# Kernel tuning notes

Measured on AMD Instinct MI355X. Metric: run time of the kernel, lower is better.

## Reference

```python
import jax, jax.numpy as jnp
import numpy as np


def _lstm_bi(x, wih, whh, b):
    # x: [B,T,D]; wih: [2,D,4H]; whh: [2,H,4H]; b: [2,4H]. PyTorch gate order i,f,g,o.
    def run(xs, wi, wh, bb):
        B, H = xs.shape[1], wh.shape[0]
        def step(carry, xt):
            h, c = carry
            g = xt @ wi + h @ wh + bb
            i, f, gg, o = jnp.split(g, 4, axis=-1)
            c = jax.nn.sigmoid(f) * c + jax.nn.sigmoid(i) * jnp.tanh(gg)
            h = jax.nn.sigmoid(o) * jnp.tanh(c)
            return (h, c), h
        z0 = jnp.zeros((B, H), xs.dtype)
        _, hs = jax.lax.scan(step, (z0, z0), xs)
        return hs
    xs = jnp.swapaxes(x, 0, 1)  # [T,B,D]
    hf = run(xs, wih[0], whh[0], b[0])
    hb = run(xs[::-1], wih[1], whh[1], b[1])[::-1]
    return jnp.swapaxes(jnp.concatenate([hf, hb], axis=-1), 0, 1)


def _norm_thr(att, thr):
    # sum-normalize, threshold-sparsify, renormalize (PSP core)
    att = att / (jnp.sum(att, -1, keepdims=True) + 1e-8)
    att = jnp.where(att > thr, att, jnp.zeros_like(att))
    return att / (jnp.sum(att, -1, keepdims=True) + 1e-8)


def _ln(x, g, b):
    mu = jnp.mean(x, -1, keepdims=True)
    var = jnp.mean(jnp.square(x - mu), -1, keepdims=True)
    return (x - mu) / jnp.sqrt(var + 1e-6) * g + b


def _forward(audio, video, thr_val, fa_w1, fa_w2, av_aw, av_ab, av_vw, av_vb,
             av_v2w, av_gw, av_hw, fv_w1, fv_w2, la_wih, la_whh, la_b,
             lv_wih, lv_whh, lv_b, vL1, vL2, aL1, aL2, vfc, afc, ln_g, ln_b, L1w, L2w):
    bs, T = audio.shape[0], audio.shape[1]
    fa = (audio @ fa_w1) @ fa_w2                          # [B,T,128]
    vf = video.reshape(bs, T, -1, video.shape[-1])        # [B,T,49,512]
    # AVGA audio-guided visual attention
    v_h = jax.nn.relu(vf @ av_vw + av_vb)                 # [B,T,49,512]
    a_h = jax.nn.relu(fa @ av_aw + av_ab)                 # [B,T,512]
    content = v_h @ av_v2w + (a_h @ av_gw)[..., None]     # [B,T,49,49]
    z = jnp.squeeze(jnp.tanh(content) @ av_hw, -1)        # [B,T,49]
    alpha = jax.nn.softmax(z, -1)
    video_t = jnp.einsum('btp,btpd->btd', alpha, vf)      # [B,T,512]
    video_t = (video_t @ fv_w1) @ fv_w2                   # [B,T,128]
    # bidirectional LSTMs
    lstm_a = _lstm_bi(fa, la_wih, la_whh, la_b)           # [B,T,256]
    lstm_v = _lstm_bi(video_t, lv_wih, lv_whh, lv_b)      # [B,T,256]
    # PSP (eval mode: dropout is identity)
    v_b1 = jax.nn.relu(lstm_v @ vL1)
    v_b2 = jax.nn.relu(lstm_v @ vL2)
    a_b1 = jax.nn.relu(lstm_a @ aL1)
    a_b2 = jax.nn.relu(lstm_a @ aL2)
    scale = 1.0 / jnp.sqrt(jnp.asarray(v_b2.shape[-1], v_b2.dtype))
    att = jax.nn.relu(jnp.einsum('bvd,bad->bva', v_b2, a_b1) * scale)  # v->a raw
    att_v2a = _norm_thr(att, thr_val)
    att_a2v = _norm_thr(jnp.swapaxes(att, 1, 2), thr_val)
    v_psp = lstm_v + jnp.einsum('bva,bad->bvd', att_v2a, a_b2)
    a_psp = lstm_a + jnp.einsum('bav,bvd->bad', att_a2v, v_b1)
    v_psp = _ln(jax.nn.relu(v_psp @ vfc), ln_g, ln_b)
    a_psp = _ln(jax.nn.relu(a_psp @ afc), ln_g, ln_b)
    fuse = 0.5 * (v_psp + a_psp)
    vn = v_psp / jnp.maximum(jnp.linalg.norm(v_psp, axis=-1, keepdims=True), 1e-12)
    an = a_psp / jnp.maximum(jnp.linalg.norm(a_psp, axis=-1, keepdims=True), 1e-12)
    cross_att = jnp.sum(vn * an, -1)                      # [B,T]
    out = jax.nn.relu(fuse @ L1w) @ L2w                   # [B,T,29]
    return (fuse, out, cross_att)


def setup_inputs() -> dict:
    key = jax.random.key(0)
    ks = iter(jax.random.split(key, 40))
    def w(*shape):
        fan_in = shape[-2] if len(shape) > 1 else shape[-1]
        return jax.random.normal(next(ks), shape, jnp.float32) * (1.0 / np.sqrt(fan_in))
    B, T = 256, 10
    return dict(
        audio=jax.random.normal(next(ks), (B, T, 128), jnp.float32),
        video=jax.random.normal(next(ks), (B, T, 7, 7, 512), jnp.float32),
        thr_val=jnp.float32(0.099),
        fa_w1=w(128, 256), fa_w2=w(256, 128),
        av_aw=w(128, 512), av_ab=jnp.zeros((512,), jnp.float32),
        av_vw=w(512, 512), av_vb=jnp.zeros((512,), jnp.float32),
        av_v2w=w(512, 49), av_gw=w(512, 49), av_hw=w(49, 1),
        fv_w1=w(512, 256), fv_w2=w(256, 128),
        la_wih=w(2, 128, 512), la_whh=w(2, 128, 512), la_b=jnp.zeros((2, 512), jnp.float32),
        lv_wih=w(2, 128, 512), lv_whh=w(2, 128, 512), lv_b=jnp.zeros((2, 512), jnp.float32),
        vL1=w(256, 256), vL2=w(256, 256), aL1=w(256, 256), aL2=w(256, 256),
        vfc=w(256, 256), afc=w(256, 256),
        ln_g=jnp.ones((256,), jnp.float32), ln_b=jnp.zeros((256,), jnp.float32),
        L1w=w(256, 64), L2w=w(64, 29),
    )


def reference(audio, video, thr_val, fa_w1, fa_w2, av_aw, av_ab, av_vw, av_vb,
              av_v2w, av_gw, av_hw, fv_w1, fv_w2, la_wih, la_whh, la_b,
              lv_wih, lv_whh, lv_b, vL1, vL2, aL1, aL2, vfc, afc, ln_g, ln_b, L1w, L2w):
    return _forward(audio, video, thr_val, fa_w1, fa_w2, av_aw, av_ab, av_vw, av_vb,
                    av_v2w, av_gw, av_hw, fv_w1, fv_w2, la_wih, la_whh, la_b,
                    lv_wih, lv_whh, lv_b, vL1, vL2, aL1, aL2, vfc, afc, ln_g, ln_b, L1w, L2w)
```

## Files before the change

kernel.cpp:

```cpp
#include <hip/hip_runtime.h>
#include <math.h>

#define DEV __device__ __forceinline__

typedef _Float16 f16x8 __attribute__((ext_vector_type(8)));
typedef _Float16 f16x4 __attribute__((ext_vector_type(4)));
typedef float    f32x4 __attribute__((ext_vector_type(4)));

DEV float sigmoidf_(float x){ return 1.0f/(1.0f + expf(-x)); }

DEV float wred64(float x){
    #pragma unroll
    for (int off=32; off; off>>=1) x += __shfl_xor(x, off);
    return x;
}

__global__ __launch_bounds__(256) void k_prep(
    const float* __restrict__ fa_w1, const float* __restrict__ fa_w2, float* __restrict__ faW,
    const float* __restrict__ fv_w1, const float* __restrict__ fv_w2, float* __restrict__ fvW,
    const float* __restrict__ av_vw, _Float16* __restrict__ Bh, _Float16* __restrict__ Bl,
    const float* __restrict__ v2w, _Float16* __restrict__ Wh, _Float16* __restrict__ Wl)
{
    int bid = blockIdx.x, t = threadIdx.x;
    if (bid < 64){
        int idx = bid*256+t; int m = idx>>7, n = idx&127;
        float acc=0.f;
        for (int k=0;k<256;k++) acc += fa_w1[m*256+k]*fa_w2[k*128+n];
        faW[idx]=acc;
    } else if (bid < 320){
        int idx = (bid-64)*256+t; int m = idx>>7, n = idx&127;
        float acc=0.f;
        for (int k=0;k<256;k++) acc += fv_w1[m*256+k]*fv_w2[k*128+n];
        fvW[idx]=acc;
    } else if (bid < 1344){
        int o = (bid-320)*256+t;
        int j = o & 7, l16 = (o>>3)&15, kg = (o>>7)&3, nf = (o>>9)&31, kt = o>>14;
        int k = kt*32 + kg*8 + j, n = nf*16 + l16;
        float x = av_vw[(size_t)k*512 + n];
        _Float16 h = (_Float16)x;
        Bh[o] = h; Bl[o] = (_Float16)(x - (float)h);
    } else {
        int o = (bid-1344)*256+t;
        int j = o & 7, l16 = (o>>3)&15, kg = (o>>7)&3, qf = (o>>9)&3, kbg = o>>11;
        int k = kbg*32 + kg*8 + j, q = qf*16 + l16;
        float x = (q < 49) ? v2w[(size_t)k*49 + q] : 0.f;
        _Float16 h = (_Float16)x;
        Wh[o] = h; Wl[o] = (_Float16)(x - (float)h);
    }
}

__global__ __launch_bounds__(256) void k_faga(
    const float* __restrict__ audio, const float* __restrict__ faW,
    const float* __restrict__ av_aw, const float* __restrict__ av_ab,
    const float* __restrict__ av_gw, float* __restrict__ fa, float* __restrict__ gGA)
{
    int b0 = blockIdx.x*4; int t = threadIdx.x;
    __shared__ float sau[4][128], sfa[4][128], sah[4][512];
    for (int i=t;i<512;i+=256){ int bt=i>>7,k=i&127; sau[bt][k]=audio[(size_t)(b0+bt)*128+k]; }
    __syncthreads();
    for (int u=0;u<2;u++){
        int i=t+u*256, bt=i>>7, n=i&127;
        float acc=0.f;
        for (int k4=0;k4<32;k4++){
            float4 x4=*(const float4*)&sau[bt][k4*4];
            acc+=x4.x*faW[(k4*4)*128+n]+x4.y*faW[(k4*4+1)*128+n]
                +x4.z*faW[(k4*4+2)*128+n]+x4.w*faW[(k4*4+3)*128+n];
        }
        sfa[bt][n]=acc; fa[(size_t)(b0+bt)*128+n]=acc;
    }
    __syncthreads();
    for (int u=0;u<2;u++){
        int n=t+u*256;
        float bv=av_ab[n];
        float acc[4]={bv,bv,bv,bv};
        for (int k4=0;k4<32;k4++){
            float w0=av_aw[(k4*4)*512+n], w1=av_aw[(k4*4+1)*512+n],
                  w2=av_aw[(k4*4+2)*512+n], w3=av_aw[(k4*4+3)*512+n];
            #pragma unroll
            for (int bt=0;bt<4;bt++){
                float4 x4=*(const float4*)&sfa[bt][k4*4];
                acc[bt]+=x4.x*w0+x4.y*w1+x4.z*w2+x4.w*w3;
            }
        }
        #pragma unroll
        for (int bt=0;bt<4;bt++) sah[bt][n]=fmaxf(acc[bt],0.f);
    }
    __syncthreads();
    if (t<196){
        int bt=t/49, q=t-bt*49;
        float acc=0.f;
        for (int k=0;k<512;k++) acc+=sah[bt][k]*av_gw[k*49+q];
        gGA[(size_t)(b0+bt)*49+q]=acc;
    }
}

DEV void cvt4_(float4 v, f16x4& hv, f16x4& lv){
    hv[0]=(_Float16)v.x; lv[0]=(_Float16)(v.x-(float)hv[0]);
    hv[1]=(_Float16)v.y; lv[1]=(_Float16)(v.y-(float)hv[1]);
    hv[2]=(_Float16)v.z; lv[2]=(_Float16)(v.z-(float)hv[2]);
    hv[3]=(_Float16)v.w; lv[3]=(_Float16)(v.w-(float)hv[3]);
}

#define MFMA16(a,b,c) __builtin_amdgcn_mfma_f32_16x16x32_f16(a,b,c,0,0,0)

__global__ __launch_bounds__(256,2) void k_avga_fused(
    const float* __restrict__ video,
    const _Float16* __restrict__ Bh, const _Float16* __restrict__ Bl,
    const float* __restrict__ bias,
    const _Float16* __restrict__ Wh, const _Float16* __restrict__ Wl,
    const float* __restrict__ gGA,
    const float* __restrict__ hw,
    float* __restrict__ vT)
{
    __shared__ __align__(16) char smem[67072];
    int bt = blockIdx.x;
    int t = threadIdx.x;
    int lane = t & 63, w = t >> 6;
    int l16 = lane & 15, lq = lane >> 4;
    int lb = lane * 16;

    int am = t >> 3, ak = (t & 7) * 4;
    int aoff1 = ((am>>4)*4 + (ak>>3))*256 + (am&15)*16 + (ak&7)*2;
    int am2 = am + 32;
    int aoff2 = ((am2>>4)*4 + (ak>>3))*256 + (am2&15)*16 + (ak&7)*2;
    size_t r1 = (size_t)bt*49 + am;  if (r1 > 125439) r1 = 125439;
    size_t r2 = (size_t)bt*49 + am2; if (r2 > 125439) r2 = 125439;
    const float* Arow1 = video + r1*512 + ak;
    const float* Arow2 = video + r2*512 + ak;

    const f32x4 vzero = {0.f,0.f,0.f,0.f};
    f32x4 acc[4][8];
    #pragma unroll
    for (int p=0;p<4;p++)
        #pragma unroll
        for (int q=0;q<8;q++) acc[p][q] = vzero;

    float4 pa0, pa1;
    pa0 = *(const float4*)(Arow1);
    pa1 = *(const float4*)(Arow2);
    {
        f16x4 hv, lv;
        char* h = &smem[0];
        cvt4_(pa0, hv, lv);
        *(f16x4*)(h + aoff1) = hv; *(f16x4*)(h + 4096 + aoff1) = lv;
        cvt4_(pa1, hv, lv);
        *(f16x4*)(h + aoff2) = hv; *(f16x4*)(h + 4096 + aoff2) = lv;
    }
    __syncthreads();

    for (int kt = 0; kt < 16; ++kt){
        int cur = kt & 1;
        bool more = (kt < 15);
        if (more){
            pa0 = *(const float4*)(Arow1 + (kt+1)*32);
            pa1 = *(const float4*)(Arow2 + (kt+1)*32);
        }
        const char* aB = &smem[cur*8192];
        f16x8 ah[4], al[4];
        #pragma unroll
        for (int p=0;p<4;p++){
            ah[p] = *(const f16x8*)(aB + p*1024 + lb);
            al[p] = *(const f16x8*)(aB + 4096 + p*1024 + lb);
        }
        #pragma unroll
        for (int q=0;q<8;q++){
            size_t bo = (size_t)kt*16384 + (size_t)(w*8 + q)*512 + lane*8;
            f16x8 bh  = *(const f16x8*)(Bh + bo);
            f16x8 bl2 = *(const f16x8*)(Bl + bo);
            #pragma unroll
            for (int p=0;p<4;p++){
                acc[p][q] = MFMA16(ah[p], bh,  acc[p][q]);
                acc[p][q] = MFMA16(ah[p], bl2, acc[p][q]);
                acc[p][q] = MFMA16(al[p], bh,  acc[p][q]);
            }
        }
        if (more){
            char* h = &smem[(cur^1)*8192];
            f16x4 hv, lv;
            cvt4_(pa0, hv, lv);
            *(f16x4*)(h + aoff1) = hv; *(f16x4*)(h + 4096 + aoff1) = lv;
            cvt4_(pa1, hv, lv);
            *(f16x4*)(h + aoff2) = hv; *(f16x4*)(h + 4096 + aoff2) = lv;
        }
        __syncthreads();
    }

    float bv[8];
    #pragma unroll
    for (int q=0;q<8;q++) bv[q] = bias[w*128 + q*16 + l16];

    char* vh = &smem[16384 + w*8192];
    f32x4 cacc[4][4];
    #pragma unroll
    for (int p=0;p<4;p++)
        #pragma unroll
        for (int qf=0;qf<4;qf++) cacc[p][qf] = vzero;

    #pragma unroll
    for (int c=0;c<4;c++){
        #pragma unroll
        for (int p=0;p<4;p++)
            #pragma unroll
            for (int qq=0;qq<2;qq++){
                int q = c*2 + qq;
                int offbase = p*1024 + (qq*2 + (l16>>3))*256 + (l16&7)*2;
                #pragma unroll
                for (int r=0;r<4;r++){
                    float x = fmaxf(acc[p][q][r] + bv[q], 0.f);
                    _Float16 hh = (_Float16)x;
                    _Float16 ll = (_Float16)(x - (float)hh);
                    int off = offbase + (lq*4 + r)*16;
                    *(_Float16*)(vh + off)        = hh;
                    *(_Float16*)(vh + 4096 + off) = ll;
                }
            }
        int kbg = w*4 + c;
        f16x8 vhh[4], vhl[4];
        #pragma unroll
        for (int p=0;p<4;p++){
            vhh[p] = *(const f16x8*)(vh + p*1024 + lb);
            vhl[p] = *(const f16x8*)(vh + 4096 + p*1024 + lb);
        }
        #pragma unroll
        for (int qf=0;qf<4;qf++){
            size_t wo = (size_t)kbg*2048 + qf*512 + lane*8;
            f16x8 wh = *(const f16x8*)(Wh + wo);
            f16x8 wl = *(const f16x8*)(Wl + wo);
            #pragma unroll
            for (int p=0;p<4;p++){
                cacc[p][qf] = MFMA16(vhh[p], wh, cacc[p][qf]);
                cacc[p][qf] = MFMA16(vhh[p], wl, cacc[p][qf]);
                cacc[p][qf] = MFMA16(vhl[p], wh, cacc[p][qf]);
            }
        }
    }

    __syncthreads();
    float* pw = (float*)&smem[w*16384];
    #pragma unroll
    for (int p=0;p<4;p++)
        #pragma unroll
        for (int qf=0;qf<4;qf++)
            #pragma unroll
            for (int r=0;r<4;r++)
                pw[(p*16 + lq*4 + r)*64 + qf*16 + l16] = cacc[p][qf][r];
    __syncthreads();
    float* cb = (float*)&smem[0];
    for (int i=t; i<4096; i+=256)
        cb[i] = cb[i] + cb[4096+i] + cb[8192+i] + cb[12288+i];
    __syncthreads();

    float* szp    = (float*)&smem[65536];
    float* salpha = (float*)&smem[66560];
    if (t < 196){
        int p = t >> 2, ds = t & 3;
        float ga = gGA[(size_t)bt*49 + p];
        float part = 0.f;
        for (int q = ds*13; q < ds*13+13 && q < 49; q++)
            part += tanhf(cb[p*64 + q] + ga) * hw[q];
        szp[t] = part;
    }
    __syncthreads();
    if (t < 64){
        float z = (t<49) ? (szp[t*4]+szp[t*4+1]+szp[t*4+2]+szp[t*4+3]) : -1e30f;
        float m = z;
        #pragma unroll
        for (int off=32; off; off>>=1) m = fmaxf(m, __shfl_xor(m, off));
        float e = (t<49)? expf(z - m) : 0.f;
        float s = e;
        #pragma unroll
        for (int off=32; off; off>>=1) s += __shfl_xor(s, off);
        salpha[t] = e / s;
    }
    __syncthreads();
    const float* vb = video + (size_t)bt*49*512;
    #pragma unroll
    for (int u=0;u<2;u++){
        int d = t + u*256;
        float a0 = 0.f;
        for (int p=0;p<49;p++) a0 += salpha[p] * vb[(size_t)p*512 + d];
        vT[(size_t)bt*512 + d] = a0;
    }
}

__global__ __launch_bounds__(256) void k_xproj2(
    const float* __restrict__ vT, const float* __restrict__ fvW,
    const float* __restrict__ fa,
    const float* __restrict__ la_wih, const float* __restrict__ la_b,
    const float* __restrict__ lv_wih, const float* __restrict__ lv_b,
    float* __restrict__ xp)
{
    int b0 = blockIdx.x*8; int t = threadIdx.x;
    __shared__ float svt[8][512];
    __shared__ float sx[2][8][128];
    for (int i=t;i<4096;i+=256){ int bt=i>>9,k=i&511; svt[bt][k]=vT[(size_t)(b0+bt)*512+k]; }
    for (int i=t;i<1024;i+=256){ int bt=i>>7,k=i&127; sx[0][bt][k]=fa[(size_t)(b0+bt)*128+k]; }
    __syncthreads();
    for (int u=0;u<4;u++){
        int i=t+u*256; int bt=i>>7, n=i&127;
        float acc=0.f;
        for (int k4=0;k4<128;k4++){
            float4 x4 = *(const float4*)&svt[bt][k4*4];
            acc += x4.x*fvW[(k4*4)*128+n] + x4.y*fvW[(k4*4+1)*128+n]
                 + x4.z*fvW[(k4*4+2)*128+n] + x4.w*fvW[(k4*4+3)*128+n];
        }
        sx[1][bt][n]=acc;
    }
    __syncthreads();
    for (int c=0;c<4;c++){
        const float* wih = ((c<2)? la_wih : lv_wih) + (size_t)(c&1)*65536;
        const float* bb  = ((c<2)? la_b   : lv_b  ) + (size_t)(c&1)*512;
        for (int u=0;u<2;u++){
            int n = t + u*256;
            float bvv = bb[n];
            float acc[8];
            #pragma unroll
            for (int bt=0;bt<8;bt++) acc[bt]=bvv;
            for (int k4=0;k4<32;k4++){
                float w0=wih[(k4*4)*512+n], w1=wih[(k4*4+1)*512+n],
                      w2=wih[(k4*4+2)*512+n], w3=wih[(k4*4+3)*512+n];
                #pragma unroll
                for (int bt=0;bt<8;bt++){
                    float4 x4 = *(const float4*)&sx[c>>1][bt][k4*4];
                    acc[bt] += x4.x*w0 + x4.y*w1 + x4.z*w2 + x4.w*w3;
                }
            }
            #pragma unroll
            for (int bt=0;bt<8;bt++)
                xp[((size_t)c*2560 + b0+bt)*512 + n] = acc[bt];
        }
    }
}

__global__ __launch_bounds__(256) void k_lstm(
    const float* __restrict__ xp, const float* __restrict__ la_whh,
    const float* __restrict__ lv_whh,
    float* __restrict__ lstm_a, float* __restrict__ lstm_v)
{
    int blk = blockIdx.x;
    int c = blk >> 6;
    int chunk = blk & 63;
    int t = threadIdx.x;
    int j  = t & 127;
    int bh = t >> 7;
    const float* whh = ((c<2)? la_whh : lv_whh) + (size_t)(c&1)*128*512;
    float* outp = (c<2)? lstm_a : lstm_v;
    int dir = c & 1;

    __shared__ float hbuf[4][128];
    float cc[2] = {0.f,0.f};
    for (int i=t;i<512;i+=256) ((float*)hbuf)[i] = 0.f;
    __syncthreads();

    for (int s=0; s<10; s++){
        int tt = dir ? (9-s) : s;
        float gi[2], gf[2], gg[2], go[2];
        #pragma unroll
        for (int b=0;b<2;b++){
            int gb = chunk*4 + bh*2 + b;
            const float* xrow = xp + ((size_t)c*2560 + gb*10 + tt)*512;
            gi[b]=xrow[j]; gf[b]=xrow[128+j]; gg[b]=xrow[256+j]; go[b]=xrow[384+j];
        }
        #pragma unroll 4
        for (int k=0;k<128;k++){
            float wi = whh[k*512 + j];
            float wf = whh[k*512 + 128 + j];
            float wg = whh[k*512 + 256 + j];
            float wo = whh[k*512 + 384 + j];
            #pragma unroll
            for (int b=0;b<2;b++){
                float hk = hbuf[bh*2+b][k];
                gi[b] += hk*wi; gf[b] += hk*wf; gg[b] += hk*wg; go[b] += hk*wo;
            }
        }
        __syncthreads();
        #pragma unroll
        for (int b=0;b<2;b++){
            float i_ = sigmoidf_(gi[b]);
            float f_ = sigmoidf_(gf[b]);
            float g_ = tanhf(gg[b]);
            float o_ = sigmoidf_(go[b]);
            cc[b] = f_*cc[b] + i_*g_;
            float h_ = o_*tanhf(cc[b]);
            hbuf[bh*2+b][j] = h_;
            int gb = chunk*4 + bh*2 + b;
            outp[((size_t)gb*10 + tt)*256 + dir*128 + j] = h_;
        }
        __syncthreads();
    }
}

__global__ __launch_bounds__(256) void k_psp1(
    const float* __restrict__ lstm_a, const float* __restrict__ lstm_v,
    const float* __restrict__ vL1, const float* __restrict__ vL2,
    const float* __restrict__ aL1, const float* __restrict__ aL2,
    float* __restrict__ vb1, float* __restrict__ vb2,
    float* __restrict__ ab1, float* __restrict__ ab2)
{
    int b0 = blockIdx.x*8; int t = threadIdx.x;
    __shared__ float sa[8][256], sv[8][256];
    for (int i=t;i<2048;i+=256){
        int bt=i>>8, k=i&255;
        sa[bt][k]=lstm_a[(size_t)(b0+bt)*256+k];
        sv[bt][k]=lstm_v[(size_t)(b0+bt)*256+k];
    }
    __syncthreads();
    float a1[8],a2[8],v1[8],v2[8];
    #pragma unroll
    for (int bt=0;bt<8;bt++){ a1[bt]=0;a2[bt]=0;v1[bt]=0;v2[bt]=0; }
    for (int k4=0;k4<64;k4++){
        #pragma unroll
        for (int j=0;j<4;j++){
            int k = k4*4+j;
            float wv1 = vL1[k*256+t], wv2 = vL2[k*256+t];
            float wa1 = aL1[k*256+t], wa2 = aL2[k*256+t];
            #pragma unroll
            for (int bt=0;bt<8;bt++){
                float xv = sv[bt][k], xa = sa[bt][k];
                v1[bt]+=xv*wv1; v2[bt]+=xv*wv2;
                a1[bt]+=xa*wa1; a2[bt]+=xa*wa2;
            }
        }
    }
    #pragma unroll
    for (int bt=0;bt<8;bt++){
        size_t o = (size_t)(b0+bt)*256+t;
        vb1[o]=fmaxf(v1[bt],0.f); vb2[o]=fmaxf(v2[bt],0.f);
        ab1[o]=fmaxf(a1[bt],0.f); ab2[o]=fmaxf(a2[bt],0.f);
    }
}

__global__ __launch_bounds__(256) void k_att(
    const float* __restrict__ lstm_a, const float* __restrict__ lstm_v,
    const float* __restrict__ vb1, const float* __restrict__ vb2,
    const float* __restrict__ ab1, const float* __restrict__ ab2,
    const float* __restrict__ thrp,
    float* __restrict__ vpsp, float* __restrict__ apsp)
{
    int b = blockIdx.x, t = threadIdx.x;
    __shared__ float sV2[2560], sA1[2560], sV1[2560], sA2[2560];
    __shared__ float satt[100], s_v2a[100], s_a2v[100];
    size_t base = (size_t)b*2560;
    for (int i=t;i<2560;i+=256){
        sV2[i]=vb2[base+i]; sA1[i]=ab1[base+i];
        sV1[i]=vb1[base+i]; sA2[i]=ab2[base+i];
    }
    __syncthreads();
    if (t < 100){
        int v = t/10, a = t - v*10;
        float acc=0.f;
        for (int k=0;k<256;k++) acc += sV2[v*256+k]*sA1[a*256+k];
        satt[t] = fmaxf(acc*(1.0f/16.0f), 0.f);
    }
    __syncthreads();
    float thr = thrp[0];
    if (t < 10){
        int v = t;
        float rs=0.f; for(int a=0;a<10;a++) rs += satt[v*10+a];
        float inv = 1.f/(rs+1e-8f);
        float tmp[10]; float rs2=0.f;
        for(int a=0;a<10;a++){ float x = satt[v*10+a]*inv; x = (x>thr)?x:0.f; tmp[a]=x; rs2+=x; }
        float inv2 = 1.f/(rs2+1e-8f);
        for(int a=0;a<10;a++) s_v2a[v*10+a] = tmp[a]*inv2;
    } else if (t>=16 && t<26){
        int a = t-16;
        float cs=0.f; for(int v=0;v<10;v++) cs += satt[v*10+a];
        float inv = 1.f/(cs+1e-8f);
        float tmp[10]; float cs2=0.f;
        for(int v=0;v<10;v++){ float x = satt[v*10+a]*inv; x=(x>thr)?x:0.f; tmp[v]=x; cs2+=x; }
        float inv2 = 1.f/(cs2+1e-8f);
        for(int v=0;v<10;v++) s_a2v[a*10+v] = tmp[v]*inv2;
    }
    __syncthreads();
    for (int v=0;v<10;v++){
        float acc = lstm_v[base + v*256 + t];
        #pragma unroll
        for (int a=0;a<10;a++) acc += s_v2a[v*10+a]*sA2[a*256+t];
        vpsp[base + v*256 + t] = acc;
    }
    for (int a=0;a<10;a++){
        float acc = lstm_a[base + a*256 + t];
        #pragma unroll
        for (int v=0;v<10;v++) acc += s_a2v[a*10+v]*sV1[v*256+t];
        apsp[base + a*256 + t] = acc;
    }
}

__global__ __launch_bounds__(256) void k_fin(
    const float* __restrict__ vpsp, const float* __restrict__ apsp,
    const float* __restrict__ vfc, const float* __restrict__ afc,
    const float* __restrict__ ln_g, const float* __restrict__ ln_b,
    const float* __restrict__ L1w, const float* __restrict__ L2w,
    float* __restrict__ dout)
{
    int b0 = blockIdx.x*8;
    int t = threadIdx.x, w = t>>6, lane = t&63;
    __shared__ float sv[8][256], sa[8][256];
    __shared__ float sfu[4][256];
    __shared__ float s64b[4][64];
    for (int i=t;i<2048;i+=256){
        int bt=i>>8, k=i&255;
        sv[bt][k]=vpsp[(size_t)(b0+bt)*256+k];
        sa[bt][k]=apsp[(size_t)(b0+bt)*256+k];
    }
    __syncthreads();
    int c0 = lane*4;
    int bt0 = w*2;
    float vv[2][4], aa[2][4];
    #pragma unroll
    for (int h=0;h<2;h++)
        #pragma unroll
        for (int jj=0;jj<4;jj++){ vv[h][jj]=0.f; aa[h][jj]=0.f; }
    for (int k=0;k<256;k++){
        float4 cv = *(const float4*)&vfc[k*256+c0];
        float4 ca = *(const float4*)&afc[k*256+c0];
        float xv0 = sv[bt0][k], xv1 = sv[bt0+1][k];
        float xa0 = sa[bt0][k], xa1 = sa[bt0+1][k];
        vv[0][0]+=xv0*cv.x; vv[0][1]+=xv0*cv.y; vv[0][2]+=xv0*cv.z; vv[0][3]+=xv0*cv.w;
        vv[1][0]+=xv1*cv.x; vv[1][1]+=xv1*cv.y; vv[1][2]+=xv1*cv.z; vv[1][3]+=xv1*cv.w;
        aa[0][0]+=xa0*ca.x; aa[0][1]+=xa0*ca.y; aa[0][2]+=xa0*ca.z; aa[0][3]+=xa0*ca.w;
        aa[1][0]+=xa1*ca.x; aa[1][1]+=xa1*ca.y; aa[1][2]+=xa1*ca.z; aa[1][3]+=xa1*ca.w;
    }
    float4 g4 = *(const float4*)&ln_g[c0];
    float4 b4 = *(const float4*)&ln_b[c0];
    float gv[4]={g4.x,g4.y,g4.z,g4.w}, bb[4]={b4.x,b4.y,b4.z,b4.w};

    for (int h=0;h<2;h++){
        int row = b0 + bt0 + h;
        float xv[4], xa[4];
        #pragma unroll
        for (int jj=0;jj<4;jj++){ xv[jj]=fmaxf(vv[h][jj],0.f); xa[jj]=fmaxf(aa[h][jj],0.f); }
        float s1 = wred64(xv[0]+xv[1]+xv[2]+xv[3]);
        float s2 = wred64(xv[0]*xv[0]+xv[1]*xv[1]+xv[2]*xv[2]+xv[3]*xv[3]);
        float mu = s1*(1.f/256.f);
        float var = s2*(1.f/256.f) - mu*mu;
        float rs = 1.f/sqrtf(var+1e-6f);
        float vln[4];
        #pragma unroll
        for (int jj=0;jj<4;jj++) vln[jj] = (xv[jj]-mu)*rs*gv[jj]+bb[jj];
        s1 = wred64(xa[0]+xa[1]+xa[2]+xa[3]);
        s2 = wred64(xa[0]*xa[0]+xa[1]*xa[1]+xa[2]*xa[2]+xa[3]*xa[3]);
        mu = s1*(1.f/256.f);
        var = s2*(1.f/256.f) - mu*mu;
        rs = 1.f/sqrtf(var+1e-6f);
        float aln[4];
        #pragma unroll
        for (int jj=0;jj<4;jj++) aln[jj] = (xa[jj]-mu)*rs*gv[jj]+bb[jj];

        float fu[4];
        #pragma unroll
        for (int jj=0;jj<4;jj++){ fu[jj] = 0.5f*(vln[jj]+aln[jj]); dout[(size_t)row*256 + c0 + jj] = fu[jj]; }

        float nv2 = wred64(vln[0]*vln[0]+vln[1]*vln[1]+vln[2]*vln[2]+vln[3]*vln[3]);
        float na2 = wred64(aln[0]*aln[0]+aln[1]*aln[1]+aln[2]*aln[2]+aln[3]*aln[3]);
        float dva = wred64(vln[0]*aln[0]+vln[1]*aln[1]+vln[2]*aln[2]+vln[3]*aln[3]);
        if (lane==0){
            float nv = fmaxf(sqrtf(nv2), 1e-12f);
            float na = fmaxf(sqrtf(na2), 1e-12f);
            dout[729600 + row] = dva/(nv*na);
        }
        *(float4*)&sfu[w][c0] = make_float4(fu[0],fu[1],fu[2],fu[3]);
        float acc = 0.f;
        for (int k4=0;k4<64;k4++){
            float4 f4 = *(const float4*)&sfu[w][k4*4];
            acc += f4.x*L1w[(k4*4)*64+lane] + f4.y*L1w[(k4*4+1)*64+lane]
                 + f4.z*L1w[(k4*4+2)*64+lane] + f4.w*L1w[(k4*4+3)*64+lane];
        }
        s64b[w][lane] = fmaxf(acc, 0.f);
        if (lane < 29){
            float acc2 = 0.f;
            #pragma unroll
            for (int k=0;k<64;k++) acc2 += s64b[w][k]*L2w[k*29+lane];
            dout[655360 + (size_t)row*29 + lane] = acc2;
        }
    }
}

extern "C" void kernel_launch(void* const* d_in, const int* in_sizes, int n_in,
                              void* d_out, int out_size, void* d_ws, size_t ws_size,
                              hipStream_t stream) {
    const float* audio  = (const float*)d_in[0];
    const float* video  = (const float*)d_in[1];
    const float* thrp   = (const float*)d_in[2];
    const float* fa_w1  = (const float*)d_in[3];
    const float* fa_w2  = (const float*)d_in[4];
    const float* av_aw  = (const float*)d_in[5];
    const float* av_ab  = (const float*)d_in[6];
    const float* av_vw  = (const float*)d_in[7];
    const float* av_vb  = (const float*)d_in[8];
    const float* av_v2w = (const float*)d_in[9];
    const float* av_gw  = (const float*)d_in[10];
    const float* av_hw  = (const float*)d_in[11];
    const float* fv_w1  = (const float*)d_in[12];
    const float* fv_w2  = (const float*)d_in[13];
    const float* la_wih = (const float*)d_in[14];
    const float* la_whh = (const float*)d_in[15];
    const float* la_b   = (const float*)d_in[16];
    const float* lv_wih = (const float*)d_in[17];
    const float* lv_whh = (const float*)d_in[18];
    const float* lv_b   = (const float*)d_in[19];
    const float* vL1    = (const float*)d_in[20];
    const float* vL2    = (const float*)d_in[21];
    const float* aL1    = (const float*)d_in[22];
    const float* aL2    = (const float*)d_in[23];
    const float* vfc    = (const float*)d_in[24];
    const float* afc    = (const float*)d_in[25];
    const float* ln_g   = (const float*)d_in[26];
    const float* ln_b   = (const float*)d_in[27];
    const float* L1w    = (const float*)d_in[28];
    const float* L2w    = (const float*)d_in[29];
    float* dout = (float*)d_out;
    float* ws = (float*)d_ws;

    float* faW  = ws;
    float* fvW  = ws + 16384;
    float* fa   = ws + 81920;
    float* gGA  = ws + 409600;
    float* vT   = ws + 535040;
    float* xp   = ws + 2173440;
    float* la   = ws + 7416320;
    float* lv   = ws + 8071680;
    float* vb1  = ws + 8727040;
    float* vb2  = ws + 9382400;
    float* ab1  = ws + 10037760;
    float* ab2  = ws + 10693120;
    float* vpsp = ws + 11348480;
    float* apsp = ws + 12003840;
    _Float16* Bh = (_Float16*)(ws + 12659200);
    _Float16* Bl = (_Float16*)(ws + 12790272);
    _Float16* Wh = (_Float16*)(ws + 12921344);
    _Float16* Wl = (_Float16*)(ws + 12937728);

    k_prep<<<1472, 256, 0, stream>>>(fa_w1, fa_w2, faW, fv_w1, fv_w2, fvW,
                                     av_vw, Bh, Bl, av_v2w, Wh, Wl);
    k_faga<<<640, 256, 0, stream>>>(audio, faW, av_aw, av_ab, av_gw, fa, gGA);
    k_avga_fused<<<2560, 256, 0, stream>>>(video, Bh, Bl, av_vb, Wh, Wl,
                                           gGA, av_hw, vT);
    k_xproj2<<<320, 256, 0, stream>>>(vT, fvW, fa, la_wih, la_b, lv_wih, lv_b, xp);
    k_lstm<<<256, 256, 0, stream>>>(xp, la_whh, lv_whh, la, lv);
    k_psp1<<<320, 256, 0, stream>>>(la, lv, vL1, vL2, aL1, aL2, vb1, vb2, ab1, ab2);
    k_att<<<256, 256, 0, stream>>>(la, lv, vb1, vb2, ab1, ab2, thrp, vpsp, apsp);
    k_fin<<<320, 256, 0, stream>>>(vpsp, apsp, vfc, afc, ln_g, ln_b, L1w, L2w, dout);
}
```

Baseline: 741.6 us.

## Move small projection GEMMs to split-fp16 MFMA kernel with packed weights

Replaces the scalar FP32 projection kernels (xproj, psp1, and the fc part of fin) with a templated MFMA GEMM. It uses hi/lo fp16 splitting for near-fp32 accuracy, with weights pre-packed into MFMA fragment layout by a new prep kernel. It also cuts AVGA shared memory by reducing the 4-wave partial sums into two buffers, which allows 3 blocks per CU. This adds more kernel launches plus a weight-packing pass that runs on every call.

New measurement: 1.212 ms. +63.4%, slower.

```diff
diff --git a/kernel.cpp b/kernel.cpp
--- a/kernel.cpp
+++ b/kernel.cpp
@@ -14,6 +14,8 @@
     for (int off=32; off; off>>=1) x += __shfl_xor(x, off);
     return x;
 }
+
+#define MFMA16(a,b,c) __builtin_amdgcn_mfma_f32_16x16x32_f16(a,b,c,0,0,0)
 
 __global__ __launch_bounds__(256) void k_prep(
     const float* __restrict__ fa_w1, const float* __restrict__ fa_w2, float* __restrict__ faW,
@@ -49,6 +51,49 @@
     }
 }
 
+DEV void packone(const float* __restrict__ src, int N, int NfrTot, int nfOff,
+                 _Float16* __restrict__ Dh, _Float16* __restrict__ Dl, int o){
+    int j = o&7, l16 = (o>>3)&15, kg = (o>>7)&3;
+    int rest = o>>9;
+    int nfl = rest % (N>>4), kt = rest / (N>>4);
+    int k = kt*32 + kg*8 + j, n = nfl*16 + l16;
+    float x = src[(size_t)k*N + n];
+    _Float16 h = (_Float16)x;
+    size_t d = ((size_t)kt*NfrTot + nfOff + nfl)*512 + kg*128 + l16*8 + j;
+    Dh[d] = h; Dl[d] = (_Float16)(x - (float)h);
+}
+
+__global__ __launch_bounds__(256) void k_prep2(
+    const float* __restrict__ fvW,
+    const float* __restrict__ la_wih, const float* __restrict__ lv_wih,
+    const float* __restrict__ vL1, const float* __restrict__ vL2,
+    const float* __restrict__ aL1, const float* __restrict__ aL2,
+    const float* __restrict__ vfc, const float* __restrict__ afc,
+    _Float16* PKfv_h, _Float16* PKfv_l,
+    _Float16* PKxa_h, _Float16* PKxa_l,
+    _Float16* PKxv_h, _Float16* PKxv_l,
+    _Float16* PKvl_h, _Float16* PKvl_l,
+    _Float16* PKal_h, _Float16* PKal_l,
+    _Float16* PKvf_h, _Float16* PKvf_l,
+    _Float16* PKaf_h, _Float16* PKaf_l)
+{
+    int seg = blockIdx.x >> 8;
+    int o = (blockIdx.x & 255)*256 + threadIdx.x;
+    switch(seg){
+    case 0:  packone(fvW,            128,  8,  0, PKfv_h, PKfv_l, o); break;
+    case 1:  packone(la_wih,         512, 64,  0, PKxa_h, PKxa_l, o); break;
+    case 2:  packone(la_wih+65536,   512, 64, 32, PKxa_h, PKxa_l, o); break;
+    case 3:  packone(lv_wih,         512, 64,  0, PKxv_h, PKxv_l, o); break;
+    case 4:  packone(lv_wih+65536,   512, 64, 32, PKxv_h, PKxv_l, o); break;
+    case 5:  packone(vL1,            256, 32,  0, PKvl_h, PKvl_l, o); break;
+    case 6:  packone(vL2,            256, 32, 16, PKvl_h, PKvl_l, o); break;
+    case 7:  packone(aL1,            256, 32,  0, PKal_h, PKal_l, o); break;
+    case 8:  packone(aL2,            256, 32, 16, PKal_h, PKal_l, o); break;
+    case 9:  packone(vfc,            256, 16,  0, PKvf_h, PKvf_l, o); break;
+    default: packone(afc,            256, 16,  0, PKaf_h, PKaf_l, o); break;
+    }
+}
+
 __global__ __launch_bounds__(256) void k_faga(
     const float* __restrict__ audio, const float* __restrict__ faW,
     const float* __restrict__ av_aw, const float* __restrict__ av_ab,
@@ -101,18 +146,15 @@
     hv[3]=(_Float16)v.w; lv[3]=(_Float16)(v.w-(float)hv[3]);
 }
 
-#define MFMA16(a,b,c) __builtin_amdgcn_mfma_f32_16x16x32_f16(a,b,c,0,0,0)
-
-__global__ __launch_bounds__(256,2) void k_avga_fused(
+__global__ __launch_bounds__(256,3) void k_avga_fused(
     const float* __restrict__ video,
     const _Float16* __restrict__ Bh, const _Float16* __restrict__ Bl,
     const float* __restrict__ bias,
     const _Float16* __restrict__ Wh, const _Float16* __restrict__ Wl,
-    const float* __restrict__ gGA,
-    const float* __restrict__ hw,
+    const float* __restrict__ gGA, const float* __restrict__ hw,
     float* __restrict__ vT)
 {
-    __shared__ __align__(16) char smem[67072];
+    __shared__ __align__(16) char smem[49152];
     int bt = blockIdx.x;
     int t = threadIdx.x;
     int lane = t & 63, w = t >> 6;
@@ -236,28 +278,38 @@
     }
 
     __syncthreads();
-    float* pw = (float*)&smem[w*16384];
-    #pragma unroll
-    for (int p=0;p<4;p++)
-        #pragma unroll
-        for (int qf=0;qf<4;qf++)
-            #pragma unroll
-            for (int r=0;r<4;r++)
-                pw[(p*16 + lq*4 + r)*64 + qf*16 + l16] = cacc[p][qf][r];
-    __syncthreads();
-    float* cb = (float*)&smem[0];
-    for (int i=t; i<4096; i+=256)
-        cb[i] = cb[i] + cb[4096+i] + cb[8192+i] + cb[12288+i];
-    __syncthreads();
-
-    float* szp    = (float*)&smem[65536];
-    float* salpha = (float*)&smem[66560];
+    float* rbuf = (float*)&smem[(w&1)*16384];
+    if (w < 2){
+        #pragma unroll
+        for (int p=0;p<4;p++)
+            #pragma unroll
+            for (int qf=0;qf<4;qf++)
+                #pragma unroll
+                for (int r=0;r<4;r++)
+                    rbuf[(p*16 + lq*4 + r)*64 + qf*16 + l16] = cacc[p][qf][r];
+    }
+    __syncthreads();
+    if (w >= 2){
+        #pragma unroll
+        for (int p=0;p<4;p++)
+            #pragma unroll
+            for (int qf=0;qf<4;qf++)
+                #pragma unroll
+                for (int r=0;r<4;r++)
+                    rbuf[(p*16 + lq*4 + r)*64 + qf*16 + l16] += cacc[p][qf][r];
+    }
+    __syncthreads();
+
+    const float* cb0 = (const float*)&smem[0];
+    const float* cb1 = (const float*)&smem[16384];
+    float* szp    = (float*)&smem[32768];
+    float* salpha = (float*)&smem[33792];
     if (t < 196){
         int p = t >> 2, ds = t & 3;
         float ga = gGA[(size_t)bt*49 + p];
         float part = 0.f;
         for (int q = ds*13; q < ds*13+13 && q < 49; q++)
-            part += tanhf(cb[p*64 + q] + ga) * hw[q];
+            part += tanhf(cb0[p*64 + q] + cb1[p*64 + q] + ga) * hw[q];
         szp[t] = part;
     }
     __syncthreads();
@@ -283,58 +335,91 @@
     }
 }
 
-__global__ __launch_bounds__(256) void k_xproj2(
-    const float* __restrict__ vT, const float* __restrict__ fvW,
-    const float* __restrict__ fa,
-    const float* __restrict__ la_wih, const float* __restrict__ la_b,
-    const float* __restrict__ lv_wih, const float* __restrict__ lv_b,
-    float* __restrict__ xp)
+template<int MP, int NQ, bool BIAS, bool RELU>
+__global__ __launch_bounds__(256) void k_gemm(
+    const float* __restrict__ A, int lda,
+    const _Float16* __restrict__ Wh, const _Float16* __restrict__ Wl,
+    const float* __restrict__ bias,
+    float* __restrict__ C, int ldc,
+    int nkt, int Nfr)
 {
-    int b0 = blockIdx.x*8; int t = threadIdx.x;
-    __shared__ float svt[8][512];
-    __shared__ float sx[2][8][128];
-    for (int i=t;i<4096;i+=256){ int bt=i>>9,k=i&511; svt[bt][k]=vT[(size_t)(b0+bt)*512+k]; }
-    for (int i=t;i<1024;i+=256){ int bt=i>>7,k=i&127; sx[0][bt][k]=fa[(size_t)(b0+bt)*128+k]; }
-    __syncthreads();
-    for (int u=0;u<4;u++){
-        int i=t+u*256; int bt=i>>7, n=i&127;
-        float acc=0.f;
-        for (int k4=0;k4<128;k4++){
-            float4 x4 = *(const float4*)&svt[bt][k4*4];
-            acc += x4.x*fvW[(k4*4)*128+n] + x4.y*fvW[(k4*4+1)*128+n]
-                 + x4.z*fvW[(k4*4+2)*128+n] + x4.w*fvW[(k4*4+3)*128+n];
-        }
-        sx[1][bt][n]=acc;
-    }
-    __syncthreads();
-    for (int c=0;c<4;c++){
-        const float* wih = ((c<2)? la_wih : lv_wih) + (size_t)(c&1)*65536;
-        const float* bb  = ((c<2)? la_b   : lv_b  ) + (size_t)(c&1)*512;
-        for (int u=0;u<2;u++){
-            int n = t + u*256;
-            float bvv = bb[n];
-            float acc[8];
-            #pragma unroll
-            for (int bt=0;bt<8;bt++) acc[bt]=bvv;
-            for (int k4=0;k4<32;k4++){
-                float w0=wih[(k4*4)*512+n], w1=wih[(k4*4+1)*512+n],
-                      w2=wih[(k4*4+2)*512+n], w3=wih[(k4*4+3)*512+n];
-                #pragma unroll
-                for (int bt=0;bt<8;bt++){
-                    float4 x4 = *(const float4*)&sx[c>>1][bt][k4*4];
-                    acc[bt] += x4.x*w0 + x4.y*w1 + x4.z*w2 + x4.w*w3;
-                }
+    __shared__ __align__(16) char sA[2][MP*2048];
+    int t = threadIdx.x, lane = t&63, w = t>>6;
+    int l16 = lane&15, lq = lane>>4, lb = lane*16;
+    int row0 = blockIdx.x * (MP*16);
+    int nf0 = blockIdx.y * (4*NQ) + w*NQ;
+
+    int am = t>>3, ak = (t&7)*4;
+    int aoff = ((am>>4)*4 + (ak>>3))*256 + (am&15)*16 + (ak&7)*2;
+    const float* Arow = A + (size_t)(row0+am)*lda + ak;
+
+    const f32x4 vzero = {0.f,0.f,0.f,0.f};
+    f32x4 acc[MP][NQ];
+    #pragma unroll
+    for (int p=0;p<MP;p++)
+        #pragma unroll
+        for (int q=0;q<NQ;q++) acc[p][q] = vzero;
+
+    float4 pa = *(const float4*)(Arow);
+    {
+        f16x4 hv, lv;
+        char* h = &sA[0][0];
+        cvt4_(pa, hv, lv);
+        *(f16x4*)(h + aoff) = hv; *(f16x4*)(h + MP*1024 + aoff) = lv;
+    }
+    __syncthreads();
+
+    for (int kt = 0; kt < nkt; ++kt){
+        int cur = kt & 1;
+        bool more = (kt+1 < nkt);
+        if (more) pa = *(const float4*)(Arow + (kt+1)*32);
+        const char* aB = &sA[cur][0];
+        f16x8 ah[MP], al[MP];
+        #pragma unroll
+        for (int p=0;p<MP;p++){
+            ah[p] = *(const f16x8*)(aB + p*1024 + lb);
+            al[p] = *(const f16x8*)(aB + MP*1024 + p*1024 + lb);
+        }
+        #pragma unroll
+        for (int q=0;q<NQ;q++){
+            size_t bo = ((size_t)kt*Nfr + nf0 + q)*512 + lane*8;
+            f16x8 bh  = *(const f16x8*)(Wh + bo);
+            f16x8 bl2 = *(const f16x8*)(Wl + bo);
+            #pragma unroll
+            for (int p=0;p<MP;p++){
+                acc[p][q] = MFMA16(ah[p], bh,  acc[p][q]);
+                acc[p][q] = MFMA16(ah[p], bl2, acc[p][q]);
+                acc[p][q] = MFMA16(al[p], bh,  acc[p][q]);
             }
-            #pragma unroll
-            for (int bt=0;bt<8;bt++)
-                xp[((size_t)c*2560 + b0+bt)*512 + n] = acc[bt];
+        }
+        if (more){
+            char* h = &sA[cur^1][0];
+            f16x4 hv, lv;
+            cvt4_(pa, hv, lv);
+            *(f16x4*)(h + aoff) = hv; *(f16x4*)(h + MP*1024 + aoff) = lv;
+        }
+        __syncthreads();
+    }
+
+    #pragma unroll
+    for (int q=0;q<NQ;q++){
+        int n = (nf0+q)*16 + l16;
+        float bv = BIAS ? bias[n] : 0.f;
+        #pragma unroll
+        for (int p=0;p<MP;p++){
+            #pragma unroll
+            for (int r=0;r<4;r++){
+                float v = acc[p][q][r] + bv;
+                if (RELU) v = fmaxf(v, 0.f);
+                C[(size_t)(row0 + p*16 + lq*4 + r)*ldc + n] = v;
+            }
         }
     }
 }
 
 __global__ __launch_bounds__(256) void k_lstm(
-    const float* __restrict__ xp, const float* __restrict__ la_whh,
-    const float* __restrict__ lv_whh,
+    const float* __restrict__ xpA, const float* __restrict__ xpV,
+    const float* __restrict__ la_whh, const float* __restrict__ lv_whh,
     float* __restrict__ lstm_a, float* __restrict__ lstm_v)
 {
     int blk = blockIdx.x;
@@ -344,6 +429,7 @@
     int j  = t & 127;
     int bh = t >> 7;
     const float* whh = ((c<2)? la_whh : lv_whh) + (size_t)(c&1)*128*512;
+    const float* xpm = (c<2)? xpA : xpV;
     float* outp = (c<2)? lstm_a : lstm_v;
     int dir = c & 1;
 
@@ -358,7 +444,7 @@
         #pragma unroll
         for (int b=0;b<2;b++){
             int gb = chunk*4 + bh*2 + b;
-            const float* xrow = xp + ((size_t)c*2560 + gb*10 + tt)*512;
+            const float* xrow = xpm + ((size_t)gb*10 + tt)*1024 + dir*512;
             gi[b]=xrow[j]; gf[b]=xrow[128+j]; gg[b]=xrow[256+j]; go[b]=xrow[384+j];
         }
         #pragma unroll 4
@@ -390,50 +476,9 @@
     }
 }
 
-__global__ __launch_bounds__(256) void k_psp1(
-    const float* __restrict__ lstm_a, const float* __restrict__ lstm_v,
-    const float* __restrict__ vL1, const float* __restrict__ vL2,
-    const float* __restrict__ aL1, const float* __restrict__ aL2,
-    float* __restrict__ vb1, float* __restrict__ vb2,
-    float* __restrict__ ab1, float* __restrict__ ab2)
-{
-    int b0 = blockIdx.x*8; int t = threadIdx.x;
-    __shared__ float sa[8][256], sv[8][256];
-    for (int i=t;i<2048;i+=256){
-        int bt=i>>8, k=i&255;
-        sa[bt][k]=lstm_a[(size_t)(b0+bt)*256+k];
-        sv[bt][k]=lstm_v[(size_t)(b0+bt)*256+k];
-    }
-    __syncthreads();
-    float a1[8],a2[8],v1[8],v2[8];
-    #pragma unroll
-    for (int bt=0;bt<8;bt++){ a1[bt]=0;a2[bt]=0;v1[bt]=0;v2[bt]=0; }
-    for (int k4=0;k4<64;k4++){
-        #pragma unroll
-        for (int j=0;j<4;j++){
-            int k = k4*4+j;
-            float wv1 = vL1[k*256+t], wv2 = vL2[k*256+t];
-            float wa1 = aL1[k*256+t], wa2 = aL2[k*256+t];
-            #pragma unroll
-            for (int bt=0;bt<8;bt++){
-                float xv = sv[bt][k], xa = sa[bt][k];
-                v1[bt]+=xv*wv1; v2[bt]+=xv*wv2;
-                a1[bt]+=xa*wa1; a2[bt]+=xa*wa2;
-            }
-        }
-    }
-    #pragma unroll
-    for (int bt=0;bt<8;bt++){
-        size_t o = (size_t)(b0+bt)*256+t;
-        vb1[o]=fmaxf(v1[bt],0.f); vb2[o]=fmaxf(v2[bt],0.f);
-        ab1[o]=fmaxf(a1[bt],0.f); ab2[o]=fmaxf(a2[bt],0.f);
-    }
-}
-
 __global__ __launch_bounds__(256) void k_att(
     const float* __restrict__ lstm_a, const float* __restrict__ lstm_v,
-    const float* __restrict__ vb1, const float* __restrict__ vb2,
-    const float* __restrict__ ab1, const float* __restrict__ ab2,
+    const float* __restrict__ vb12, const float* __restrict__ ab12,
     const float* __restrict__ thrp,
     float* __restrict__ vpsp, float* __restrict__ apsp)
 {
@@ -442,8 +487,10 @@
     __shared__ float satt[100], s_v2a[100], s_a2v[100];
     size_t base = (size_t)b*2560;
     for (int i=t;i<2560;i+=256){
-        sV2[i]=vb2[base+i]; sA1[i]=ab1[base+i];
-        sV1[i]=vb1[base+i]; sA2[i]=ab2[base+i];
+        int rr = i>>8, cc2 = i&255;
+        size_t ro = (size_t)(b*10 + rr)*512;
+        sV1[i]=vb12[ro + cc2]; sV2[i]=vb12[ro + 256 + cc2];
+        sA1[i]=ab12[ro + cc2]; sA2[i]=ab12[ro + 256 + cc2];
     }
     __syncthreads();
     if (t < 100){
@@ -487,49 +534,26 @@
 }
 
 __global__ __launch_bounds__(256) void k_fin(
-    const float* __restrict__ vpsp, const float* __restrict__ apsp,
-    const float* __restrict__ vfc, const float* __restrict__ afc,
+    const float* __restrict__ vrl, const float* __restrict__ arl,
     const float* __restrict__ ln_g, const float* __restrict__ ln_b,
     const float* __restrict__ L1w, const float* __restrict__ L2w,
     float* __restrict__ dout)
 {
     int b0 = blockIdx.x*8;
     int t = threadIdx.x, w = t>>6, lane = t&63;
-    __shared__ float sv[8][256], sa[8][256];
     __shared__ float sfu[4][256];
     __shared__ float s64b[4][64];
-    for (int i=t;i<2048;i+=256){
-        int bt=i>>8, k=i&255;
-        sv[bt][k]=vpsp[(size_t)(b0+bt)*256+k];
-        sa[bt][k]=apsp[(size_t)(b0+bt)*256+k];
-    }
-    __syncthreads();
     int c0 = lane*4;
     int bt0 = w*2;
-    float vv[2][4], aa[2][4];
-    #pragma unroll
-    for (int h=0;h<2;h++)
-        #pragma unroll
-        for (int jj=0;jj<4;jj++){ vv[h][jj]=0.f; aa[h][jj]=0.f; }
-    for (int k=0;k<256;k++){
-        float4 cv = *(const float4*)&vfc[k*256+c0];
-        float4 ca = *(const float4*)&afc[k*256+c0];
-        float xv0 = sv[bt0][k], xv1 = sv[bt0+1][k];
-        float xa0 = sa[bt0][k], xa1 = sa[bt0+1][k];
-        vv[0][0]+=xv0*cv.x; vv[0][1]+=xv0*cv.y; vv[0][2]+=xv0*cv.z; vv[0][3]+=xv0*cv.w;
-        vv[1][0]+=xv1*cv.x; vv[1][1]+=xv1*cv.y; vv[1][2]+=xv1*cv.z; vv[1][3]+=xv1*cv.w;
-        aa[0][0]+=xa0*ca.x; aa[0][1]+=xa0*ca.y; aa[0][2]+=xa0*ca.z; aa[0][3]+=xa0*ca.w;
-        aa[1][0]+=xa1*ca.x; aa[1][1]+=xa1*ca.y; aa[1][2]+=xa1*ca.z; aa[1][3]+=xa1*ca.w;
-    }
     float4 g4 = *(const float4*)&ln_g[c0];
     float4 b4 = *(const float4*)&ln_b[c0];
     float gv[4]={g4.x,g4.y,g4.z,g4.w}, bb[4]={b4.x,b4.y,b4.z,b4.w};
 
     for (int h=0;h<2;h++){
         int row = b0 + bt0 + h;
-        float xv[4], xa[4];
-        #pragma unroll
-        for (int jj=0;jj<4;jj++){ xv[jj]=fmaxf(vv[h][jj],0.f); xa[jj]=fmaxf(aa[h][jj],0.f); }
+        float4 xv4 = *(const float4*)&vrl[(size_t)row*256 + c0];
+        float4 xa4 = *(const float4*)&arl[(size_t)row*256 + c0];
+        float xv[4]={xv4.x,xv4.y,xv4.z,xv4.w}, xa[4]={xa4.x,xa4.y,xa4.z,xa4.w};
         float s1 = wred64(xv[0]+xv[1]+xv[2]+xv[3]);
         float s2 = wred64(xv[0]*xv[0]+xv[1]*xv[1]+xv[2]*xv[2]+xv[3]*xv[3]);
         float mu = s1*(1.f/256.f);
@@ -617,28 +641,61 @@
     float* fa   = ws + 81920;
     float* gGA  = ws + 409600;
     float* vT   = ws + 535040;
-    float* xp   = ws + 2173440;
+    float* xpA  = ws + 2173440;
+    float* xpV  = ws + 4794880;
     float* la   = ws + 7416320;
     float* lv   = ws + 8071680;
-    float* vb1  = ws + 8727040;
-    float* vb2  = ws + 9382400;
-    float* ab1  = ws + 10037760;
-    float* ab2  = ws + 10693120;
+    float* vb12 = ws + 8727040;
+    float* ab12 = ws + 10037760;
     float* vpsp = ws + 11348480;
     float* apsp = ws + 12003840;
     _Float16* Bh = (_Float16*)(ws + 12659200);
     _Float16* Bl = (_Float16*)(ws + 12790272);
     _Float16* Wh = (_Float16*)(ws + 12921344);
     _Float16* Wl = (_Float16*)(ws + 12937728);
+    _Float16* PKfv_h = (_Float16*)(ws + 12954112);
+    _Float16* PKfv_l = (_Float16*)(ws + 12986880);
+    _Float16* PKxa_h = (_Float16*)(ws + 13019648);
+    _Float16* PKxa_l = (_Float16*)(ws + 13085184);
+    _Float16* PKxv_h = (_Float16*)(ws + 13150720);
+    _Float16* PKxv_l = (_Float16*)(ws + 13216256);
+    _Float16* PKvl_h = (_Float16*)(ws + 13281792);
+    _Float16* PKvl_l = (_Float16*)(ws + 13347328);
+    _Float16* PKal_h = (_Float16*)(ws + 13412864);
+    _Float16* PKal_l = (_Float16*)(ws + 13478400);
+    _Float16* PKvf_h = (_Float16*)(ws + 13543936);
+    _Float16* PKvf_l = (_Float16*)(ws + 13576704);
+    _Float16* PKaf_h = (_Float16*)(ws + 13609472);
+    _Float16* PKaf_l = (_Float16*)(ws + 13642240);
+    float* vfea = ws + 13675008;
+    float* vrl  = ws + 14002688;
+    float* arl  = ws + 14658048;
 
     k_prep<<<1472, 256, 0, stream>>>(fa_w1, fa_w2, faW, fv_w1, fv_w2, fvW,
                                      av_vw, Bh, Bl, av_v2w, Wh, Wl);
+    k_prep2<<<2816, 256, 0, stream>>>(fvW, la_wih, lv_wih, vL1, vL2, aL1, aL2,
+                                      vfc, afc,
+                                      PKfv_h, PKfv_l, PKxa_h, PKxa_l, PKxv_h, PKxv_l,
+                                      PKvl_h, PKvl_l, PKal_h, PKal_l,
+                                      PKvf_h, PKvf_l, PKaf_h, PKaf_l);
     k_faga<<<640, 256, 0, stream>>>(audio, faW, av_aw, av_ab, av_gw, fa, gGA);
     k_avga_fused<<<2560, 256, 0, stream>>>(video, Bh, Bl, av_vb, Wh, Wl,
                                            gGA, av_hw, vT);
-    k_xproj2<<<320, 256, 0, stream>>>(vT, fvW, fa, la_wih, la_b, lv_wih, lv_b, xp);
-    k_lstm<<<256, 256, 0, stream>>>(xp, la_whh, lv_whh, la, lv);
-    k_psp1<<<320, 256, 0, stream>>>(la, lv, vL1, vL2, aL1, aL2, vb1, vb2, ab1, ab2);
-    k_att<<<256, 256, 0, stream>>>(la, lv, vb1, vb2, ab1, ab2, thrp, vpsp, apsp);
-    k_fin<<<320, 256, 0, stream>>>(vpsp, apsp, vfc, afc, ln_g, ln_b, L1w, L2w, dout);
-}
+    k_gemm<2,2,false,false><<<dim3(80,1), 256, 0, stream>>>(
+        vT, 512, PKfv_h, PKfv_l, nullptr, vfea, 128, 16, 8);
+    k_gemm<2,4,true,false><<<dim3(80,4), 256, 0, stream>>>(
+        fa, 128, PKxa_h, PKxa_l, la_b, xpA, 1024, 4, 64);
+    k_gemm<2,4,true,false><<<dim3(80,4), 256, 0, stream>>>(
+        vfea, 128, PKxv_h, PKxv_l, lv_b, xpV, 1024, 4, 64);
+    k_lstm<<<256, 256, 0, stream>>>(xpA, xpV, la_whh, lv_whh, la, lv);
+    k_gemm<2,4,false,true><<<dim3(80,2), 256, 0, stream>>>(
+        lv, 256, PKvl_h, PKvl_l, nullptr, vb12, 512, 8, 32);
+    k_gemm<2,4,false,true><<<dim3(80,2), 256, 0, stream>>>(
+        la, 256, PKal_h, PKal_l, nullptr, ab12, 512, 8, 32);
+    k_att<<<256, 256, 0, stream>>>(la, lv, vb12, ab12, thrp, vpsp, apsp);
+    k_gemm<2,4,false,true><<<dim3(80,1), 256, 0, stream>>>(
+        vpsp, 256, PKvf_h, PKvf_l, nullptr, vrl, 256, 8, 16);
+    k_gemm<2,4,false,true><<<dim3(80,1), 256, 0, stream>>>(
+        apsp, 256, PKaf_h, PKaf_l, nullptr, arl, 256, 8, 16);
+    k_fin<<<320, 256, 0, stream>>>(vrl, arl, ln_g, ln_b, L1w, L2w, dout);
+}
```
